# Performance work log

Measured on AMD Instinct MI355X. Metric: run time of the kernel, lower is better.

Reference implementation:

```python
import jax, jax.numpy as jnp
import numpy as np

B, S, D, H, WIN = 2, 2048, 1024, 16, 128
DH = D // H


def setup_inputs() -> dict:
    key = jax.random.key(0)
    ks = jax.random.split(key, 6)
    sc = D ** -0.5
    return {
        "x": jax.random.normal(ks[0], (B, S, D), jnp.float32),
        "in_proj_w": jax.random.normal(ks[1], (3 * D, D), jnp.float32) * sc,
        "in_proj_b": jnp.zeros((3 * D,), jnp.float32),
        "out_proj_w": jax.random.normal(ks[2], (D, D), jnp.float32) * sc,
        "out_proj_b": jnp.zeros((D,), jnp.float32),
        "ln1_g": jnp.ones((D,), jnp.float32),
        "ln1_b": jnp.zeros((D,), jnp.float32),
        "spec_wr": jax.random.normal(ks[3], (S // 2 + 1, D), jnp.float32) * 0.02 + 1.0,
        "spec_wi": jax.random.normal(ks[4], (S // 2 + 1, D), jnp.float32) * 0.02,
        "ln2_g": jnp.ones((D,), jnp.float32),
        "ln2_b": jnp.zeros((D,), jnp.float32),
    }


def _layernorm(x, g, b, eps=1e-5):
    mu = jnp.mean(x, axis=-1, keepdims=True)
    var = jnp.mean(jnp.square(x - mu), axis=-1, keepdims=True)
    return (x - mu) * jax.lax.rsqrt(var + eps) * g + b


def reference(x, in_proj_w, in_proj_b, out_proj_w, out_proj_b,
              ln1_g, ln1_b, spec_wr, spec_wi, ln2_g, ln2_b):
    b, s, d = x.shape
    # --- sliding-window MHA (torch nn.MultiheadAttention math) ---
    qkv = x @ in_proj_w.T + in_proj_b            # [B,S,3D]
    q, k, v = jnp.split(qkv, 3, axis=-1)
    q = q.reshape(b, s, H, DH)
    k = k.reshape(b, s, H, DH)
    v = v.reshape(b, s, H, DH)
    scores = jnp.einsum('bqhd,bkhd->bhqk', q, k) * (DH ** -0.5)
    idx = jnp.arange(s)
    band_mask = jnp.abs(idx[:, None] - idx[None, :]) > WIN  # True = masked
    scores = jnp.where(band_mask[None, None], -jnp.inf, scores)
    probs = jax.nn.softmax(scores, axis=-1)
    attn = jnp.einsum('bhqk,bkhd->bqhd', probs, v).reshape(b, s, d)
    attn_out = attn @ out_proj_w.T + out_proj_b
    x_attn = _layernorm(x + attn_out, ln1_g, ln1_b)
    # --- spectral block: rfft along seq, learned complex filter, irfft ---
    Xf = jnp.fft.rfft(x, axis=1)                  # [B, S//2+1, D] complex
    Wc = spec_wr + 1j * spec_wi
    x_wave = jnp.fft.irfft(Xf * Wc[None], n=s, axis=1).astype(x.dtype)
    # --- mix ---
    return _layernorm(x_attn + x_wave, ln2_g, ln2_b)
```

## Files before the change

kernel.cpp:

```cpp
#include <hip/hip_runtime.h>
#include <hip/hip_bf16.h>
#include <math.h>

#define BB    2
#define SS    2048
#define DD    1024
#define HH    16
#define DHH   64
#define WINW  128
#define MROWS (BB * SS)

typedef __attribute__((ext_vector_type(8))) short short8;
typedef __attribute__((ext_vector_type(4))) short short4v;
typedef __attribute__((ext_vector_type(4))) float floatx4;

__device__ __forceinline__ float bf2f(short s) {
  union { unsigned u; float f; } t;
  t.u = ((unsigned)(unsigned short)s) << 16;
  return t.f;
}

__global__ __launch_bounds__(256) void transpose_x_cast(
    const float* __restrict__ src, float* __restrict__ dstT,
    __hip_bfloat16* __restrict__ dst_bf) {
  __shared__ float tile[64][65];
  const size_t base = (size_t)blockIdx.z * SS * DD;
  const int c0 = blockIdx.x * 64;
  const int r0 = blockIdx.y * 64;
  const int tx = threadIdx.x & 63;
  const int ty = threadIdx.x >> 6;
#pragma unroll
  for (int i = 0; i < 16; ++i) {
    const int r = ty * 16 + i;
    const float v = src[base + (size_t)(r0 + r) * DD + c0 + tx];
    tile[r][tx] = v;
    dst_bf[base + (size_t)(r0 + r) * DD + c0 + tx] = __float2bfloat16(v);
  }
  __syncthreads();
#pragma unroll
  for (int i = 0; i < 16; ++i) {
    const int c = ty * 16 + i;
    dstT[base + (size_t)(c0 + c) * SS + r0 + tx] = tile[tx][c];
  }
}

__global__ __launch_bounds__(256) void cast_w(
    const float* __restrict__ w_in, const float* __restrict__ w_out,
    __hip_bfloat16* __restrict__ o_in, __hip_bfloat16* __restrict__ o_out) {
  const int i = (blockIdx.x * 256 + threadIdx.x) * 4;
  const float* src; __hip_bfloat16* dst; int j;
  if (i < 3 * DD * DD) { src = w_in; dst = o_in; j = i; }
  else { src = w_out; dst = o_out; j = i - 3 * DD * DD; }
  const float4 v = *(const float4*)(src + j);
  dst[j + 0] = __float2bfloat16(v.x);
  dst[j + 1] = __float2bfloat16(v.y);
  dst[j + 2] = __float2bfloat16(v.z);
  dst[j + 3] = __float2bfloat16(v.w);
}

__global__ __launch_bounds__(256) void transpose_wrwi_bf(
    const float* __restrict__ wr, const float* __restrict__ wi,
    __hip_bfloat16* __restrict__ wrT, __hip_bfloat16* __restrict__ wiT) {
  __shared__ float tile[64][65];
  const float* src = blockIdx.z ? wi : wr;
  __hip_bfloat16* dst = blockIdx.z ? wiT : wrT;
  const int R = 1025, C = DD;
  const int c0 = blockIdx.x * 64;
  const int r0 = blockIdx.y * 64;
  const int tx = threadIdx.x & 63;
  const int ty = threadIdx.x >> 6;
#pragma unroll
  for (int i = 0; i < 16; ++i) {
    const int r = ty * 16 + i;
    if (r0 + r < R) tile[r][tx] = src[(size_t)(r0 + r) * C + c0 + tx];
  }
  __syncthreads();
#pragma unroll
  for (int i = 0; i < 16; ++i) {
    const int c = ty * 16 + i;
    if (r0 + tx < R) dst[(size_t)(c0 + c) * R + r0 + tx] = __float2bfloat16(tile[tx][c]);
  }
}

__device__ inline void load16_lds(const __hip_bfloat16* g, __hip_bfloat16* l) {
  __builtin_amdgcn_global_load_lds(
      (const __attribute__((address_space(1))) uint32_t*)g,
      (__attribute__((address_space(3))) uint32_t*)l, 16, 0, 0);
}

template <bool BF16OUT>
__device__ __forceinline__ void gemm_tile128(
    const __hip_bfloat16* __restrict__ A, const __hip_bfloat16* __restrict__ B,
    const float* __restrict__ bias, void* __restrict__ Cp,
    int N, int K, int row0, int col0,
    __hip_bfloat16* As, __hip_bfloat16* Bs) {
  const int tid  = threadIdx.x;
  const int lane = tid & 63;
  const int wave = tid >> 6;
  const int wrow = (wave >> 1) * 64;
  const int wcol = (wave & 1) * 64;
  const int srow = tid >> 2;
  const int skk  = (tid & 3) * 8;
  const int quad = lane >> 4;
  const int l16  = lane & 15;
  floatx4 acc[4][4] = {};
  for (int k0 = 0; k0 < K; k0 += 32) {
    __syncthreads();
    load16_lds(A + (size_t)(row0 + srow) * K + k0 + skk,      &As[tid * 8]);
    load16_lds(A + (size_t)(row0 + 64 + srow) * K + k0 + skk, &As[2048 + tid * 8]);
    load16_lds(B + (size_t)(col0 + srow) * K + k0 + skk,      &Bs[tid * 8]);
    load16_lds(B + (size_t)(col0 + 64 + srow) * K + k0 + skk, &Bs[2048 + tid * 8]);
    __syncthreads();
    short8 af[4], bf[4];
#pragma unroll
    for (int i = 0; i < 4; ++i)
      af[i] = *(const short8*)&As[(wrow + i * 16 + l16) * 32 + quad * 8];
#pragma unroll
    for (int j = 0; j < 4; ++j)
      bf[j] = *(const short8*)&Bs[(wcol + j * 16 + l16) * 32 + quad * 8];
#pragma unroll
    for (int i = 0; i < 4; ++i)
#pragma unroll
      for (int j = 0; j < 4; ++j)
        acc[i][j] = __builtin_amdgcn_mfma_f32_16x16x32_bf16(af[i], bf[j], acc[i][j], 0, 0, 0);
  }
#pragma unroll
  for (int i = 0; i < 4; ++i) {
#pragma unroll
    for (int j = 0; j < 4; ++j) {
      const int col = col0 + wcol + j * 16 + l16;
      const float bs = bias[col];
#pragma unroll
      for (int r = 0; r < 4; ++r) {
        const int row = row0 + wrow + i * 16 + quad * 4 + r;
        if (BF16OUT)
          ((__hip_bfloat16*)Cp)[(size_t)row * N + col] = __float2bfloat16(acc[i][j][r] + bs);
        else
          ((float*)Cp)[(size_t)row * N + col] = acc[i][j][r] + bs;
      }
    }
  }
}

#define PADI(a) ((a) + ((a) >> 5))

__device__ __forceinline__ void spec_body(
    int sid, float* __restrict__ xT,
    const __hip_bfloat16* __restrict__ wrT, const __hip_bfloat16* __restrict__ wiT,
    float* sm) {
  float* re = sm;
  float* im = sm + 2112;
  const int tid = threadIdx.x;
  const int dpair = sid & 511;
  const int b = sid >> 9;
  const int d0 = dpair * 2, d1 = d0 + 1;
  float* col0 = xT + ((size_t)b * DD + d0) * SS;
  float* col1 = xT + ((size_t)b * DD + d1) * SS;

  for (int s4 = tid * 4; s4 < SS; s4 += 1024) {
    const float4 a = *(const float4*)(col0 + s4);
    const float4 c = *(const float4*)(col1 + s4);
    const int p = PADI(s4);
    re[p] = a.x; re[p + 1] = a.y; re[p + 2] = a.z; re[p + 3] = a.w;
    im[p] = c.x; im[p + 1] = c.y; im[p + 2] = c.z; im[p + 3] = c.w;
  }

  for (int stage = 11; stage >= 1; --stage) {
    __syncthreads();
    const int half = 1 << (stage - 1);
    const float ang0 = -6.283185307179586f / (float)(1 << stage);
#pragma unroll 4
    for (int t = tid; t < SS / 2; t += 256) {
      const int gI = t >> (stage - 1);
      const int p = t & (half - 1);
      const int i = (gI << stage) + p;
      const int j = i + half;
      float sn, cs;
      __sincosf(ang0 * (float)p, &sn, &cs);
      const int ii = PADI(i), jj = PADI(j);
      const float ar = re[ii], ai = im[ii], br = re[jj], bi = im[jj];
      re[ii] = ar + br; im[ii] = ai + bi;
      const float dr = ar - br, di = ai - bi;
      re[jj] = dr * cs - di * sn;
      im[jj] = dr * sn + di * cs;
    }
  }
  __syncthreads();

  const __hip_bfloat16* w0r = wrT + (size_t)d0 * 1025;
  const __hip_bfloat16* w0i = wiT + (size_t)d0 * 1025;
  const __hip_bfloat16* w1r = wrT + (size_t)d1 * 1025;
  const __hip_bfloat16* w1i = wiT + (size_t)d1 * 1025;
  const float sc = 1.0f / (float)SS;
  for (int k = tid; k < 1024; k += 256) {
    if (k == 0) {
      re[0] *= __bfloat162float(w0r[0]) * sc;
      im[0] *= __bfloat162float(w1r[0]) * sc;
      re[1] *= __bfloat162float(w0r[1024]) * sc;
      im[1] *= __bfloat162float(w1r[1024]) * sc;
    } else {
      const int p1 = PADI(__brev((unsigned)k) >> 21);
      const int p2 = PADI(__brev((unsigned)(SS - k)) >> 21);
      const float ra = re[p1], ia = im[p1];
      const float rb = re[p2], ib = im[p2];
      const float z0r = 0.5f * (ra + rb), z0i = 0.5f * (ia - ib);
      const float z1r = 0.5f * (ia + ib), z1i = -0.5f * (ra - rb);
      const float a0 = __bfloat162float(w0r[k]) * sc, b0 = __bfloat162float(w0i[k]) * sc;
      const float a1 = __bfloat162float(w1r[k]) * sc, b1 = __bfloat162float(w1i[k]) * sc;
      const float y0r = z0r * a0 - z0i * b0, y0i = z0r * b0 + z0i * a0;
      const float y1r = z1r * a1 - z1i * b1, y1i = z1r * b1 + z1i * a1;
      re[p1] = y0r - y1i; im[p1] = y0i + y1r;
      re[p2] = y0r + y1i; im[p2] = y1r - y0i;
    }
  }

  for (int stage = 1; stage <= 11; ++stage) {
    __syncthreads();
    const int half = 1 << (stage - 1);
    const float ang0 = 6.283185307179586f / (float)(1 << stage);
#pragma unroll 4
    for (int t = tid; t < SS / 2; t += 256) {
      const int gI = t >> (stage - 1);
      const int p = t & (half - 1);
      const int i = (gI << stage) + p;
      const int j = i + half;
      float sn, cs;
      __sincosf(ang0 * (float)p, &sn, &cs);
      const int ii = PADI(i), jj = PADI(j);
      const float br = re[jj], bi = im[jj];
      const float tr = br * cs - bi * sn;
      const float ti = br * sn + bi * cs;
      const float ar = re[ii], ai = im[ii];
      re[ii] = ar + tr; im[ii] = ai + ti;
      re[jj] = ar - tr; im[jj] = ai - ti;
    }
  }
  __syncthreads();

  for (int s4 = tid * 4; s4 < SS; s4 += 1024) {
    const int p = PADI(s4);
    float4 a, c;
    a.x = re[p]; a.y = re[p + 1]; a.z = re[p + 2]; a.w = re[p + 3];
    c.x = im[p]; c.y = im[p + 1]; c.z = im[p + 2]; c.w = im[p + 3];
    *(float4*)(col0 + s4) = a;
    *(float4*)(col1 + s4) = c;
  }
}

__global__ __launch_bounds__(256) void gemm1_spec(
    const __hip_bfloat16* __restrict__ x_bf, const __hip_bfloat16* __restrict__ w_in_bf,
    const float* __restrict__ in_b, __hip_bfloat16* __restrict__ qkv_bf,
    float* __restrict__ xT, const __hip_bfloat16* __restrict__ wrT,
    const __hip_bfloat16* __restrict__ wiT) {
  extern __shared__ __align__(16) char smem[];
  if (blockIdx.x < 768) {
    const int id = blockIdx.x;
    const int col0 = (id % 24) * 128;
    const int row0 = (id / 24) * 128;
    gemm_tile128<true>(x_bf, w_in_bf, in_b, qkv_bf, 3 * DD, DD, row0, col0,
                       (__hip_bfloat16*)smem, (__hip_bfloat16*)smem + 4096);
  } else {
    spec_body(blockIdx.x - 768, xT, wrT, wiT, (float*)smem);
  }
}

__global__ __launch_bounds__(256) void gemm2_tback(
    const __hip_bfloat16* __restrict__ attn_bf, const __hip_bfloat16* __restrict__ w_out_bf,
    const float* __restrict__ out_b, __hip_bfloat16* __restrict__ attn_out_bf,
    const float* __restrict__ xT, __hip_bfloat16* __restrict__ x_wave_bf) {
  extern __shared__ __align__(16) char smem[];
  if (blockIdx.x < 256) {
    const int id = blockIdx.x;
    const int col0 = (id % 8) * 128;
    const int row0 = (id / 8) * 128;
    gemm_tile128<true>(attn_bf, w_out_bf, out_b, attn_out_bf, DD, DD, row0, col0,
                       (__hip_bfloat16*)smem, (__hip_bfloat16*)smem + 4096);
  } else {
    float (*tile)[65] = (float(*)[65])smem;
    const int id = blockIdx.x - 256;
    const int bz = id >> 9;
    const int rem = id & 511;
    const int s0 = (rem >> 4) * 64;
    const int d0 = (rem & 15) * 64;
    const int tx = threadIdx.x & 63;
    const int ty = threadIdx.x >> 6;
    const float* src = xT + (size_t)bz * DD * SS;
    __hip_bfloat16* dst = x_wave_bf + (size_t)bz * SS * DD;
#pragma unroll
    for (int i = 0; i < 16; ++i) {
      const int r = ty * 16 + i;
      tile[r][tx] = src[(size_t)(d0 + r) * SS + s0 + tx];
    }
    __syncthreads();
#pragma unroll
    for (int i = 0; i < 16; ++i) {
      const int c = ty * 16 + i;
      dst[(size_t)(s0 + c) * DD + d0 + tx] = __float2bfloat16(tile[tx][c]);
    }
  }
}

__global__ __launch_bounds__(256, 2) void attn_mfma(
    const __hip_bfloat16* __restrict__ qkv, __hip_bfloat16* __restrict__ attn) {
  __shared__ __attribute__((aligned(16))) __hip_bfloat16 QsA[64 * 32];
  __shared__ __attribute__((aligned(16))) __hip_bfloat16 QsB[64 * 32];
  __shared__ __attribute__((aligned(16))) __hip_bfloat16 KsA[160 * 32];
  __shared__ __attribute__((aligned(16))) __hip_bfloat16 KsB[160 * 32];
  __shared__ __attribute__((aligned(16))) __hip_bfloat16 Vt[64 * 168];
  __shared__ __attribute__((aligned(16))) __hip_bfloat16 Ps[64 * 168];

  const int tid  = threadIdx.x;
  const int lane = tid & 63;
  const int w    = tid >> 6;
  const int quad = lane >> 4;
  const int l16  = lane & 15;
  const int q0   = blockIdx.x * 64;
  const int h    = blockIdx.y;
  const int b    = blockIdx.z;
  const int kbase = q0 - WINW;

  const int r_ = tid >> 2;
  const int c8 = (tid & 3) * 8;

  {
    const __hip_bfloat16* src = qkv + ((size_t)(b * SS + q0 + r_)) * (3 * DD) + h * DHH;
    load16_lds(src + c8,      &QsA[r_ * 32 + c8]);
    load16_lds(src + 32 + c8, &QsB[r_ * 32 + c8]);
  }

  short8 qf0, qf1;
  float m_run[4] = {-1e30f, -1e30f, -1e30f, -1e30f};
  float l_run[4] = {0.f, 0.f, 0.f, 0.f};
  floatx4 ob[4] = {};

  for (int c = 0; c < 2; ++c) {
    const int ck0 = kbase + c * 160;
    __syncthreads();
#pragma unroll
    for (int it = 0; it < 3; ++it) {
      const int r = it * 64 + r_;
      if (r < 160) {
        int key = ck0 + r; key = key < 0 ? 0 : (key > SS - 1 ? SS - 1 : key);
        const __hip_bfloat16* src = qkv + ((size_t)(b * SS + key)) * (3 * DD) + DD + h * DHH;
        load16_lds(src + c8,      &KsA[r * 32 + c8]);
        load16_lds(src + 32 + c8, &KsB[r * 32 + c8]);
      }
    }
    {
      const int k4 = (tid >> 3) * 4;
      const int d8 = (tid & 7) * 8;
#pragma unroll
      for (int it = 0; it < 2; ++it) {
        const int rr = it * 128 + k4;
        if (rr < 160) {
          short8 v[4];
#pragma unroll
          for (int u = 0; u < 4; ++u) {
            int key = ck0 + rr + u; key = key < 0 ? 0 : (key > SS - 1 ? SS - 1 : key);
            v[u] = *(const short8*)(qkv + ((size_t)(b * SS + key)) * (3 * DD) + 2 * DD + h * DHH + d8);
          }
#pragma unroll
          for (int j = 0; j < 8; ++j) {
            short4v pk; pk[0] = v[0][j]; pk[1] = v[1][j]; pk[2] = v[2][j]; pk[3] = v[3][j];
            *(short4v*)&Vt[(d8 + j) * 168 + rr] = pk;
          }
        }
      }
    }
    __syncthreads();

    if (c == 0) {
      qf0 = *(const short8*)&QsA[(w * 16 + l16) * 32 + quad * 8];
      qf1 = *(const short8*)&QsB[(w * 16 + l16) * 32 + quad * 8];
    }

    floatx4 sc[10];
#pragma unroll
    for (int kt = 0; kt < 10; ++kt) {
      const short8 bk0 = *(const short8*)&KsA[(kt * 16 + l16) * 32 + quad * 8];
      const short8 bk1 = *(const short8*)&KsB[(kt * 16 + l16) * 32 + quad * 8];
      floatx4 a = {};
      a = __builtin_amdgcn_mfma_f32_16x16x32_bf16(qf0, bk0, a, 0, 0, 0);
      a = __builtin_amdgcn_mfma_f32_16x16x32_bf16(qf1, bk1, a, 0, 0, 0);
      sc[kt] = a;
    }

    float cm[4] = {-1e30f, -1e30f, -1e30f, -1e30f};
#pragma unroll
    for (int kt = 0; kt < 10; ++kt) {
      const int key = ck0 + kt * 16 + l16;
#pragma unroll
      for (int r = 0; r < 4; ++r) {
        const int qq = q0 + w * 16 + quad * 4 + r;
        const int dqk = qq - key;
        const bool ok = (key >= 0) & (key < SS) & (dqk <= WINW) & (dqk >= -WINW);
        const float s = ok ? sc[kt][r] * 0.125f : -1e30f;
        sc[kt][r] = s;
        cm[r] = fmaxf(cm[r], s);
      }
    }
#pragma unroll
    for (int off = 1; off < 16; off <<= 1)
#pragma unroll
      for (int r = 0; r < 4; ++r) cm[r] = fmaxf(cm[r], __shfl_xor(cm[r], off, 64));

    float alpha[4], csum[4] = {0.f, 0.f, 0.f, 0.f};
#pragma unroll
    for (int r = 0; r < 4; ++r) {
      const float mn = fmaxf(m_run[r], cm[r]);
      alpha[r] = __expf(m_run[r] - mn);
      m_run[r] = mn;
    }

    __hip_bfloat16* Pw = &Ps[w * 16 * 168];
#pragma unroll
    for (int kt = 0; kt < 10; ++kt) {
#pragma unroll
      for (int r = 0; r < 4; ++r) {
        const float p = __expf(sc[kt][r] - m_run[r]);
        csum[r] += p;
        Pw[(quad * 4 + r) * 168 + kt * 16 + l16] = __float2bfloat16(p);
      }
    }
#pragma unroll
    for (int off = 1; off < 16; off <<= 1)
#pragma unroll
      for (int r = 0; r < 4; ++r) csum[r] += __shfl_xor(csum[r], off, 64);
#pragma unroll
    for (int r = 0; r < 4; ++r) l_run[r] = l_run[r] * alpha[r] + csum[r];
#pragma unroll
    for (int t = 0; t < 4; ++t)
#pragma unroll
      for (int r = 0; r < 4; ++r) ob[t][r] *= alpha[r];

#pragma unroll
    for (int kt = 0; kt < 5; ++kt) {
      const short8 pf = *(const short8*)&Pw[l16 * 168 + kt * 32 + quad * 8];
#pragma unroll
      for (int t = 0; t < 4; ++t) {
        const short8 vf = *(const short8*)&Vt[(t * 16 + l16) * 168 + kt * 32 + quad * 8];
        ob[t] = __builtin_amdgcn_mfma_f32_16x16x32_bf16(pf, vf, ob[t], 0, 0, 0);
      }
    }
  }

  float inv[4];
#pragma unroll
  for (int r = 0; r < 4; ++r) inv[r] = 1.f / l_run[r];
  const int qq0 = q0 + w * 16 + quad * 4;
#pragma unroll
  for (int t = 0; t < 4; ++t)
#pragma unroll
    for (int r = 0; r < 4; ++r)
      attn[((size_t)(b * SS + qq0 + r)) * DD + h * DHH + t * 16 + l16] =
          __float2bfloat16(ob[t][r] * inv[r]);
}

__global__ __launch_bounds__(256) void ln_fused(
    const float* __restrict__ x, const __hip_bfloat16* __restrict__ attn_out,
    const float* __restrict__ g1, const float* __restrict__ b1,
    const __hip_bfloat16* __restrict__ xwave,
    const float* __restrict__ g2, const float* __restrict__ b2,
    float* __restrict__ out) {
  const int row = blockIdx.x;
  const int tid = threadIdx.x;
  const int lane = tid & 63;
  const int wave = tid >> 6;
  __shared__ float red[8];

  const float4 xv = *(const float4*)(x + (size_t)row * DD + tid * 4);
  const short4v av = *(const short4v*)(attn_out + (size_t)row * DD + tid * 4);
  float v[4] = {xv.x + bf2f(av[0]), xv.y + bf2f(av[1]),
                xv.z + bf2f(av[2]), xv.w + bf2f(av[3])};

  float s = v[0] + v[1] + v[2] + v[3];
  float s2 = v[0] * v[0] + v[1] * v[1] + v[2] * v[2] + v[3] * v[3];
#pragma unroll
  for (int off = 32; off; off >>= 1) {
    s += __shfl_xor(s, off, 64);
    s2 += __shfl_xor(s2, off, 64);
  }
  if (lane == 0) { red[wave] = s; red[4 + wave] = s2; }
  __syncthreads();
  s = red[0] + red[1] + red[2] + red[3];
  s2 = red[4] + red[5] + red[6] + red[7];
  float mu = s * (1.f / DD);
  float var = s2 * (1.f / DD) - mu * mu;
  float r = rsqrtf(var + 1e-5f);

  const float4 g1v = *(const float4*)(g1 + tid * 4);
  const float4 b1v = *(const float4*)(b1 + tid * 4);
  const short4v wv = *(const short4v*)(xwave + (size_t)row * DD + tid * 4);
  float a[4];
  a[0] = (v[0] - mu) * r * g1v.x + b1v.x + bf2f(wv[0]);
  a[1] = (v[1] - mu) * r * g1v.y + b1v.y + bf2f(wv[1]);
  a[2] = (v[2] - mu) * r * g1v.z + b1v.z + bf2f(wv[2]);
  a[3] = (v[3] - mu) * r * g1v.w + b1v.w + bf2f(wv[3]);

  s = a[0] + a[1] + a[2] + a[3];
  s2 = a[0] * a[0] + a[1] * a[1] + a[2] * a[2] + a[3] * a[3];
#pragma unroll
  for (int off = 32; off; off >>= 1) {
    s += __shfl_xor(s, off, 64);
    s2 += __shfl_xor(s2, off, 64);
  }
  __syncthreads();
  if (lane == 0) { red[wave] = s; red[4 + wave] = s2; }
  __syncthreads();
  s = red[0] + red[1] + red[2] + red[3];
  s2 = red[4] + red[5] + red[6] + red[7];
  mu = s * (1.f / DD);
  var = s2 * (1.f / DD) - mu * mu;
  r = rsqrtf(var + 1e-5f);

  const float4 g2v = *(const float4*)(g2 + tid * 4);
  const float4 b2v = *(const float4*)(b2 + tid * 4);
  float4 o;
  o.x = (a[0] - mu) * r * g2v.x + b2v.x;
  o.y = (a[1] - mu) * r * g2v.y + b2v.y;
  o.z = (a[2] - mu) * r * g2v.z + b2v.z;
  o.w = (a[3] - mu) * r * g2v.w + b2v.w;
  *(float4*)(out + (size_t)row * DD + tid * 4) = o;
}

extern "C" void kernel_launch(void* const* d_in, const int* in_sizes, int n_in,
                              void* d_out, int out_size, void* d_ws, size_t ws_size,
                              hipStream_t stream) {
  const float* x     = (const float*)d_in[0];
  const float* in_w  = (const float*)d_in[1];
  const float* in_b  = (const float*)d_in[2];
  const float* out_w = (const float*)d_in[3];
  const float* out_b = (const float*)d_in[4];
  const float* ln1_g = (const float*)d_in[5];
  const float* ln1_b = (const float*)d_in[6];
  const float* wr    = (const float*)d_in[7];
  const float* wi    = (const float*)d_in[8];
  const float* ln2_g = (const float*)d_in[9];
  const float* ln2_b = (const float*)d_in[10];
  float* out = (float*)d_out;

  char* ws = (char*)d_ws;
  float* xT                = (float*)(ws);
  __hip_bfloat16* x_bf     = (__hip_bfloat16*)(ws + 16777216);
  __hip_bfloat16* attn_bf  = (__hip_bfloat16*)(ws + 16777216);
  __hip_bfloat16* w_in_bf  = (__hip_bfloat16*)(ws + 25165824);
  __hip_bfloat16* w_out_bf = (__hip_bfloat16*)(ws + 31457280);
  __hip_bfloat16* qkv_bf   = (__hip_bfloat16*)(ws + 33554432);
  __hip_bfloat16* attn_out_bf = (__hip_bfloat16*)(ws + 33554432);
  __hip_bfloat16* x_wave_bf   = (__hip_bfloat16*)(ws + 44040192);
  __hip_bfloat16* wrT      = (__hip_bfloat16*)(ws + 58720256);
  __hip_bfloat16* wiT      = (__hip_bfloat16*)(ws + 60819456);

  transpose_x_cast<<<dim3(16, 32, 2), 256, 0, stream>>>(x, xT, x_bf);

  cast_w<<<4096, 256, 0, stream>>>(in_w, out_w, w_in_bf, w_out_bf);

  transpose_wrwi_bf<<<dim3(16, 17, 2), 256, 0, stream>>>(wr, wi, wrT, wiT);

  gemm1_spec<<<1792, 256, 16896, stream>>>(x_bf, w_in_bf, in_b, qkv_bf,
                                           xT, wrT, wiT);

  attn_mfma<<<dim3(SS / 64, HH, BB), 256, 0, stream>>>(qkv_bf, attn_bf);

  gemm2_tback<<<1280, 256, 16640, stream>>>(attn_bf, w_out_bf, out_b,
                                            attn_out_bf, xT, x_wave_bf);

  ln_fused<<<MROWS, 256, 0, stream>>>(x, attn_out_bf, ln1_g, ln1_b,
                                      x_wave_bf, ln2_g, ln2_b, out);
}
```

Before: 232.6 us.

## Merge prep kernels into one launch and deepen GEMM K-step to 64

Three preprocessing kernels (x transpose/cast, weight cast, spectral weight transpose) are merged into a single launch that dispatches on block index, removing two launch gaps. The GEMM tile now loads two 32-wide K slabs per barrier pair, halving the number of syncs per K loop. In exchange, shared memory for the GEMM and spectral kernels grows to 32KB, which may reduce occupancy.

```diff
diff --git a/kernel.cpp b/kernel.cpp
--- a/kernel.cpp
+++ b/kernel.cpp
@@ -20,80 +20,89 @@
   return t.f;
 }
 
-__global__ __launch_bounds__(256) void transpose_x_cast(
-    const float* __restrict__ src, float* __restrict__ dstT,
-    __hip_bfloat16* __restrict__ dst_bf) {
-  __shared__ float tile[64][65];
-  const size_t base = (size_t)blockIdx.z * SS * DD;
-  const int c0 = blockIdx.x * 64;
-  const int r0 = blockIdx.y * 64;
-  const int tx = threadIdx.x & 63;
-  const int ty = threadIdx.x >> 6;
-#pragma unroll
-  for (int i = 0; i < 16; ++i) {
-    const int r = ty * 16 + i;
-    const float v = src[base + (size_t)(r0 + r) * DD + c0 + tx];
-    tile[r][tx] = v;
-    dst_bf[base + (size_t)(r0 + r) * DD + c0 + tx] = __float2bfloat16(v);
-  }
-  __syncthreads();
-#pragma unroll
-  for (int i = 0; i < 16; ++i) {
-    const int c = ty * 16 + i;
-    dstT[base + (size_t)(c0 + c) * SS + r0 + tx] = tile[tx][c];
-  }
-}
-
-__global__ __launch_bounds__(256) void cast_w(
-    const float* __restrict__ w_in, const float* __restrict__ w_out,
-    __hip_bfloat16* __restrict__ o_in, __hip_bfloat16* __restrict__ o_out) {
-  const int i = (blockIdx.x * 256 + threadIdx.x) * 4;
-  const float* src; __hip_bfloat16* dst; int j;
-  if (i < 3 * DD * DD) { src = w_in; dst = o_in; j = i; }
-  else { src = w_out; dst = o_out; j = i - 3 * DD * DD; }
-  const float4 v = *(const float4*)(src + j);
-  dst[j + 0] = __float2bfloat16(v.x);
-  dst[j + 1] = __float2bfloat16(v.y);
-  dst[j + 2] = __float2bfloat16(v.z);
-  dst[j + 3] = __float2bfloat16(v.w);
-}
-
-__global__ __launch_bounds__(256) void transpose_wrwi_bf(
-    const float* __restrict__ wr, const float* __restrict__ wi,
-    __hip_bfloat16* __restrict__ wrT, __hip_bfloat16* __restrict__ wiT) {
-  __shared__ float tile[64][65];
-  const float* src = blockIdx.z ? wi : wr;
-  __hip_bfloat16* dst = blockIdx.z ? wiT : wrT;
-  const int R = 1025, C = DD;
-  const int c0 = blockIdx.x * 64;
-  const int r0 = blockIdx.y * 64;
-  const int tx = threadIdx.x & 63;
-  const int ty = threadIdx.x >> 6;
-#pragma unroll
-  for (int i = 0; i < 16; ++i) {
-    const int r = ty * 16 + i;
-    if (r0 + r < R) tile[r][tx] = src[(size_t)(r0 + r) * C + c0 + tx];
-  }
-  __syncthreads();
-#pragma unroll
-  for (int i = 0; i < 16; ++i) {
-    const int c = ty * 16 + i;
-    if (r0 + tx < R) dst[(size_t)(c0 + c) * R + r0 + tx] = __float2bfloat16(tile[tx][c]);
-  }
-}
-
 __device__ inline void load16_lds(const __hip_bfloat16* g, __hip_bfloat16* l) {
   __builtin_amdgcn_global_load_lds(
       (const __attribute__((address_space(1))) uint32_t*)g,
       (__attribute__((address_space(3))) uint32_t*)l, 16, 0, 0);
 }
 
+__global__ __launch_bounds__(256) void prep_fused(
+    const float* __restrict__ x, float* __restrict__ xT,
+    __hip_bfloat16* __restrict__ x_bf,
+    const float* __restrict__ w_in, const float* __restrict__ w_out,
+    __hip_bfloat16* __restrict__ w_in_bf, __hip_bfloat16* __restrict__ w_out_bf,
+    const float* __restrict__ wr, const float* __restrict__ wi,
+    __hip_bfloat16* __restrict__ wrT, __hip_bfloat16* __restrict__ wiT) {
+  __shared__ float tile[64][65];
+  const int id = blockIdx.x;
+  const int tx = threadIdx.x & 63;
+  const int ty = threadIdx.x >> 6;
+
+  if (id < 1024) {
+    const int bz = id >> 9;
+    const int rem = id & 511;
+    const int c0 = (rem & 15) * 64;
+    const int r0 = (rem >> 4) * 64;
+    const size_t base = (size_t)bz * SS * DD;
+#pragma unroll
+    for (int i = 0; i < 16; ++i) {
+      const int r = ty * 16 + i;
+      const float v = x[base + (size_t)(r0 + r) * DD + c0 + tx];
+      tile[r][tx] = v;
+      x_bf[base + (size_t)(r0 + r) * DD + c0 + tx] = __float2bfloat16(v);
+    }
+    __syncthreads();
+#pragma unroll
+    for (int i = 0; i < 16; ++i) {
+      const int c = ty * 16 + i;
+      xT[base + (size_t)(c0 + c) * SS + r0 + tx] = tile[tx][c];
+    }
+  } else if (id < 2048) {
+    const int blk = id - 1024;
+    const float* src; __hip_bfloat16* dst; size_t off;
+    if (blk < 768) { src = w_in; dst = w_in_bf; off = (size_t)blk * 4096; }
+    else { src = w_out; dst = w_out_bf; off = (size_t)(blk - 768) * 4096; }
+#pragma unroll
+    for (int c = 0; c < 4; ++c) {
+      const size_t j = off + c * 1024 + threadIdx.x * 4;
+      const float4 v = *(const float4*)(src + j);
+      dst[j + 0] = __float2bfloat16(v.x);
+      dst[j + 1] = __float2bfloat16(v.y);
+      dst[j + 2] = __float2bfloat16(v.z);
+      dst[j + 3] = __float2bfloat16(v.w);
+    }
+  } else {
+    const int id2 = id - 2048;
+    const int half = id2 >= 272;
+    const int rem = id2 - (half ? 272 : 0);
+    const float* src = half ? wi : wr;
+    __hip_bfloat16* dst = half ? wiT : wrT;
+    const int R = 1025, C = DD;
+    const int c0 = (rem & 15) * 64;
+    const int r0 = (rem >> 4) * 64;
+#pragma unroll
+    for (int i = 0; i < 16; ++i) {
+      const int r = ty * 16 + i;
+      if (r0 + r < R) tile[r][tx] = src[(size_t)(r0 + r) * C + c0 + tx];
+    }
+    __syncthreads();
+#pragma unroll
+    for (int i = 0; i < 16; ++i) {
+      const int c = ty * 16 + i;
+      if (r0 + tx < R) dst[(size_t)(c0 + c) * R + r0 + tx] = __float2bfloat16(tile[tx][c]);
+    }
+  }
+}
+
 template <bool BF16OUT>
 __device__ __forceinline__ void gemm_tile128(
     const __hip_bfloat16* __restrict__ A, const __hip_bfloat16* __restrict__ B,
     const float* __restrict__ bias, void* __restrict__ Cp,
-    int N, int K, int row0, int col0,
-    __hip_bfloat16* As, __hip_bfloat16* Bs) {
+    int N, int K, int row0, int col0, __hip_bfloat16* sm) {
+  __hip_bfloat16* As0 = sm;
+  __hip_bfloat16* As1 = sm + 4096;
+  __hip_bfloat16* Bs0 = sm + 8192;
+  __hip_bfloat16* Bs1 = sm + 12288;
   const int tid  = threadIdx.x;
   const int lane = tid & 63;
   const int wave = tid >> 6;
@@ -104,25 +113,45 @@
   const int quad = lane >> 4;
   const int l16  = lane & 15;
   floatx4 acc[4][4] = {};
-  for (int k0 = 0; k0 < K; k0 += 32) {
-    __syncthreads();
-    load16_lds(A + (size_t)(row0 + srow) * K + k0 + skk,      &As[tid * 8]);
-    load16_lds(A + (size_t)(row0 + 64 + srow) * K + k0 + skk, &As[2048 + tid * 8]);
-    load16_lds(B + (size_t)(col0 + srow) * K + k0 + skk,      &Bs[tid * 8]);
-    load16_lds(B + (size_t)(col0 + 64 + srow) * K + k0 + skk, &Bs[2048 + tid * 8]);
-    __syncthreads();
-    short8 af[4], bf[4];
-#pragma unroll
-    for (int i = 0; i < 4; ++i)
-      af[i] = *(const short8*)&As[(wrow + i * 16 + l16) * 32 + quad * 8];
-#pragma unroll
-    for (int j = 0; j < 4; ++j)
-      bf[j] = *(const short8*)&Bs[(wcol + j * 16 + l16) * 32 + quad * 8];
-#pragma unroll
-    for (int i = 0; i < 4; ++i)
+  for (int k0 = 0; k0 < K; k0 += 64) {
+    __syncthreads();
+    load16_lds(A + (size_t)(row0 + srow) * K + k0 + skk,           &As0[tid * 8]);
+    load16_lds(A + (size_t)(row0 + 64 + srow) * K + k0 + skk,      &As0[2048 + tid * 8]);
+    load16_lds(A + (size_t)(row0 + srow) * K + k0 + 32 + skk,      &As1[tid * 8]);
+    load16_lds(A + (size_t)(row0 + 64 + srow) * K + k0 + 32 + skk, &As1[2048 + tid * 8]);
+    load16_lds(B + (size_t)(col0 + srow) * K + k0 + skk,           &Bs0[tid * 8]);
+    load16_lds(B + (size_t)(col0 + 64 + srow) * K + k0 + skk,      &Bs0[2048 + tid * 8]);
+    load16_lds(B + (size_t)(col0 + srow) * K + k0 + 32 + skk,      &Bs1[tid * 8]);
+    load16_lds(B + (size_t)(col0 + 64 + srow) * K + k0 + 32 + skk, &Bs1[2048 + tid * 8]);
+    __syncthreads();
+    {
+      short8 af[4], bf[4];
+#pragma unroll
+      for (int i = 0; i < 4; ++i)
+        af[i] = *(const short8*)&As0[(wrow + i * 16 + l16) * 32 + quad * 8];
 #pragma unroll
       for (int j = 0; j < 4; ++j)
-        acc[i][j] = __builtin_amdgcn_mfma_f32_16x16x32_bf16(af[i], bf[j], acc[i][j], 0, 0, 0);
+        bf[j] = *(const short8*)&Bs0[(wcol + j * 16 + l16) * 32 + quad * 8];
+#pragma unroll
+      for (int i = 0; i < 4; ++i)
+#pragma unroll
+        for (int j = 0; j < 4; ++j)
+          acc[i][j] = __builtin_amdgcn_mfma_f32_16x16x32_bf16(af[i], bf[j], acc[i][j], 0, 0, 0);
+    }
+    {
+      short8 af[4], bf[4];
+#pragma unroll
+      for (int i = 0; i < 4; ++i)
+        af[i] = *(const short8*)&As1[(wrow + i * 16 + l16) * 32 + quad * 8];
+#pragma unroll
+      for (int j = 0; j < 4; ++j)
+        bf[j] = *(const short8*)&Bs1[(wcol + j * 16 + l16) * 32 + quad * 8];
+#pragma unroll
+      for (int i = 0; i < 4; ++i)
+#pragma unroll
+        for (int j = 0; j < 4; ++j)
+          acc[i][j] = __builtin_amdgcn_mfma_f32_16x16x32_bf16(af[i], bf[j], acc[i][j], 0, 0, 0);
+    }
   }
 #pragma unroll
   for (int i = 0; i < 4; ++i) {
@@ -258,7 +287,7 @@
     const int col0 = (id % 24) * 128;
     const int row0 = (id / 24) * 128;
     gemm_tile128<true>(x_bf, w_in_bf, in_b, qkv_bf, 3 * DD, DD, row0, col0,
-                       (__hip_bfloat16*)smem, (__hip_bfloat16*)smem + 4096);
+                       (__hip_bfloat16*)smem);
   } else {
     spec_body(blockIdx.x - 768, xT, wrT, wiT, (float*)smem);
   }
@@ -274,7 +303,7 @@
     const int col0 = (id % 8) * 128;
     const int row0 = (id / 8) * 128;
     gemm_tile128<true>(attn_bf, w_out_bf, out_b, attn_out_bf, DD, DD, row0, col0,
-                       (__hip_bfloat16*)smem, (__hip_bfloat16*)smem + 4096);
+                       (__hip_bfloat16*)smem);
   } else {
     float (*tile)[65] = (float(*)[65])smem;
     const int id = blockIdx.x - 256;
@@ -551,18 +580,15 @@
   __hip_bfloat16* wrT      = (__hip_bfloat16*)(ws + 58720256);
   __hip_bfloat16* wiT      = (__hip_bfloat16*)(ws + 60819456);
 
-  transpose_x_cast<<<dim3(16, 32, 2), 256, 0, stream>>>(x, xT, x_bf);
-
-  cast_w<<<4096, 256, 0, stream>>>(in_w, out_w, w_in_bf, w_out_bf);
-
-  transpose_wrwi_bf<<<dim3(16, 17, 2), 256, 0, stream>>>(wr, wi, wrT, wiT);
-
-  gemm1_spec<<<1792, 256, 16896, stream>>>(x_bf, w_in_bf, in_b, qkv_bf,
+  prep_fused<<<2592, 256, 0, stream>>>(x, xT, x_bf, in_w, out_w,
+                                       w_in_bf, w_out_bf, wr, wi, wrT, wiT);
+
+  gemm1_spec<<<1792, 256, 32768, stream>>>(x_bf, w_in_bf, in_b, qkv_bf,
                                            xT, wrT, wiT);
 
   attn_mfma<<<dim3(SS / 64, HH, BB), 256, 0, stream>>>(qkv_bf, attn_bf);
 
-  gemm2_tback<<<1280, 256, 16640, stream>>>(attn_bf, w_out_bf, out_b,
+  gemm2_tback<<<1280, 256, 32768, stream>>>(attn_bf, w_out_bf, out_b,
                                             attn_out_bf, xT, x_wave_bf);
 
   ln_fused<<<MROWS, 256, 0, stream>>>(x, attn_out_bf, ln1_g, ln1_b,
```

New measurement: 230.5 us. About the same (-0.9%).
